# Performance work log

Hardware: AMD Instinct MI355X
Metric: run time of the kernel (lower is better)

## Reference

```python
import jax, jax.numpy as jnp
import numpy as np

N = 131072        # total nodes in batched graph
E = 2097152       # total edges (avg degree 16)
F_IN = 256        # input feature dim
DIMS = [64, 32, 16]
G = 128           # number of graphs in batch


def setup_inputs() -> dict:
    key = jax.random.key(0)
    ks = jax.random.split(key, 16)
    inp = {
        "features": jax.random.normal(ks[0], (N, F_IN), jnp.float32),
        "src": jax.random.randint(ks[1], (E,), 0, N),
        "dst": jax.random.randint(ks[2], (E,), 0, N),
        "graph_ids": jnp.sort(jax.random.randint(ks[3], (N,), 0, G)),
    }
    d = F_IN
    for i, out in enumerate(DIMS):
        inp[f"W{i}"] = jax.random.normal(ks[4 + 2 * i], (d, out), jnp.float32) / np.sqrt(d).astype(np.float32)
        inp[f"b{i}"] = jax.random.normal(ks[5 + 2 * i], (out,), jnp.float32) * 0.01
        d = out
    inp["Wc"] = jax.random.normal(ks[10], (DIMS[-1], 1), jnp.float32) / np.sqrt(DIMS[-1]).astype(np.float32)
    inp["bc"] = jax.random.normal(ks[11], (1,), jnp.float32) * 0.01
    return inp


def _graph_conv(h, W, b, src, dst, src_norm, dst_norm):
    # DGL GraphConv, norm='both', activation=relu, allow_zero_in_degree=True
    # (in_feats > out_feats everywhere here, so project before aggregating)
    hw = (h * src_norm) @ W                       # [N, out]
    agg = jax.ops.segment_sum(hw[src], dst, num_segments=N)  # gather->scatter-add
    return jax.nn.relu(agg * dst_norm + b)


def reference(features, src, dst, graph_ids, W0, b0, W1, b1, W2, b2, Wc, bc):
    ones_e = jnp.ones((E,), jnp.float32)
    out_deg = jax.ops.segment_sum(ones_e, src, num_segments=N)
    in_deg = jax.ops.segment_sum(ones_e, dst, num_segments=N)
    # DGL clamps degrees to >=1 before pow(-0.5)
    src_norm = jnp.power(jnp.maximum(out_deg, 1.0), -0.5)[:, None]  # [N,1]
    dst_norm = jnp.power(jnp.maximum(in_deg, 1.0), -0.5)[:, None]

    h = features
    for W, b in ((W0, b0), (W1, b1), (W2, b2)):
        h = _graph_conv(h, W, b, src, dst, src_norm, dst_norm)

    # dgl.mean_nodes over batched graph
    sums = jax.ops.segment_sum(h, graph_ids, num_segments=G)          # [G,16]
    cnt = jax.ops.segment_sum(jnp.ones((N,), jnp.float32), graph_ids, num_segments=G)
    hg = sums / jnp.maximum(cnt, 1.0)[:, None]

    return (hg @ Wc + bc).squeeze(-1)  # [G] logits
```

## Files before the change

### kernel.cpp

```cpp
#include <hip/hip_runtime.h>

#define N_NODES 131072
#define N_EDGES 2097152
#define N_GRAPHS 128
#define POOL_NPB 256
#define NB 256
#define BUCKET_SHIFT 9
#define BUCKET_CAP 9728
#define BIN_EPT 32

__global__ __launch_bounds__(256) void k_init_buckets(int* __restrict__ cursor_d,
                                                      int* __restrict__ cursor_s) {
  int i = threadIdx.x;
  cursor_d[i] = i * BUCKET_CAP;
  cursor_s[i] = i * BUCKET_CAP;
}

__global__ __launch_bounds__(256) void k_bin(const int* __restrict__ src,
                                             const int* __restrict__ dst,
                                             int* __restrict__ cursor_d,
                                             int* __restrict__ cursor_s,
                                             unsigned int* __restrict__ recs_d,
                                             unsigned short* __restrict__ recs_s) {
  __shared__ int hd[NB];
  __shared__ int hs[NB];
  const int t = threadIdx.x;
  const int e0 = blockIdx.x * (256 * BIN_EPT);
  hd[t] = 0; hs[t] = 0;
  __syncthreads();
#pragma unroll 4
  for (int k = 0; k < BIN_EPT; ++k) {
    int e = e0 + k * 256 + t;
    atomicAdd(&hd[dst[e] >> BUCKET_SHIFT], 1);
    atomicAdd(&hs[src[e] >> BUCKET_SHIFT], 1);
  }
  __syncthreads();
  { int c = hd[t]; hd[t] = c ? atomicAdd(&cursor_d[t], c) : 0; }
  { int c = hs[t]; hs[t] = c ? atomicAdd(&cursor_s[t], c) : 0; }
  __syncthreads();
#pragma unroll 4
  for (int k = 0; k < BIN_EPT; ++k) {
    int e = e0 + k * 256 + t;
    int s = src[e];
    int d = dst[e];
    int pd = atomicAdd(&hd[d >> BUCKET_SHIFT], 1);
    recs_d[pd] = ((unsigned int)s << BUCKET_SHIFT) | (unsigned int)(d & 511);
    int ps = atomicAdd(&hs[s >> BUCKET_SHIFT], 1);
    recs_s[ps] = (unsigned short)(s & 511);
  }
}

__global__ __launch_bounds__(512) void k_outdeg(const unsigned short* __restrict__ recs_s,
                                                const int* __restrict__ cursor_s,
                                                float* __restrict__ src_norm) {
  __shared__ int hist[512];
  const int b = blockIdx.x;
  const int t = threadIdx.x;
  hist[t] = 0;
  __syncthreads();
  const int beg = b * BUCKET_CAP;
  const int end = cursor_s[b];
  for (int i = beg + t; i < end; i += 512) atomicAdd(&hist[recs_s[i]], 1);
  __syncthreads();
  int od = hist[t]; if (od < 1) od = 1;
  src_norm[b * 512 + t] = 1.0f / sqrtf((float)od);
}

__global__ __launch_bounds__(256) void k_bucket_scan(const int* __restrict__ cursor_d,
                                                     int* __restrict__ bucket_base,
                                                     int* __restrict__ row_start) {
  __shared__ int tmp[256];
  int t = threadIdx.x;
  int c = cursor_d[t] - t * BUCKET_CAP;
  tmp[t] = c;
  __syncthreads();
  for (int off = 1; off < 256; off <<= 1) {
    int x = (t >= off) ? tmp[t - off] : 0;
    __syncthreads();
    tmp[t] += x;
    __syncthreads();
  }
  bucket_base[t] = tmp[t] - c;
  if (t == 0) row_start[N_NODES] = N_EDGES;
}

__global__ __launch_bounds__(512) void k_fill2(const unsigned int* __restrict__ recs_d,
                                               const int* __restrict__ cursor_d,
                                               const int* __restrict__ bucket_base,
                                               int* __restrict__ row_start,
                                               float* __restrict__ dst_norm,
                                               int* __restrict__ csr_src) {
  __shared__ int hist[512];
  __shared__ int lcur[512];
  const int b = blockIdx.x;
  const int t = threadIdx.x;
  hist[t] = 0;
  __syncthreads();
  const int beg = b * BUCKET_CAP;
  const int end = cursor_d[b];
  for (int i = beg + t; i < end; i += 512) atomicAdd(&hist[recs_d[i] & 511], 1);
  __syncthreads();
  int deg = hist[t];
  lcur[t] = deg;
  __syncthreads();
  for (int off = 1; off < 512; off <<= 1) {
    int x = (t >= off) ? lcur[t - off] : 0;
    __syncthreads();
    lcur[t] += x;
    __syncthreads();
  }
  int rs = bucket_base[b] + lcur[t] - deg;
  row_start[b * 512 + t] = rs;
  int dd = deg < 1 ? 1 : deg;
  dst_norm[b * 512 + t] = 1.0f / sqrtf((float)dd);
  lcur[t] = rs;
  __syncthreads();
  for (int i = beg + t; i < end; i += 512) {
    unsigned int r = recs_d[i];
    int p = atomicAdd(&lcur[r & 511], 1);
    csr_src[p] = (int)(r >> BUCKET_SHIFT);
  }
}

template <int DIN, int DOUT>
__global__ __launch_bounds__(256) void k_gemm(const float* __restrict__ h,
                                              const float* __restrict__ src_norm,
                                              const float* __restrict__ W,
                                              float* __restrict__ out) {
  constexpr int KC   = 32;
  constexpr int ROWS = 64;
  constexpr int TN   = DOUT / 16;
  constexpr int WEL  = KC * DOUT;
  __shared__ float hT[KC][ROWS];
  __shared__ float Ws[KC][DOUT];

  const int t  = threadIdx.x;
  const int rowBase = blockIdx.x * ROWS;
  const int tr = t & 15;
  const int tc = t >> 4;
  const int rg0 = (t >> 3) & 31;
  const int ph  = t >> 8;
  const int ks  = (t & 7) * 4;

  float acc[4][TN];
#pragma unroll
  for (int i = 0; i < 4; ++i)
#pragma unroll
    for (int j = 0; j < TN; ++j) acc[i][j] = 0.0f;

  for (int kc = 0; kc < DIN; kc += KC) {
#pragma unroll
    for (int p = 0; p < 2; ++p) {
      int rg = rg0 + 32 * p;
      float4 v = *reinterpret_cast<const float4*>(&h[(size_t)(rowBase + rg) * DIN + kc + ks]);
      hT[ks + 0][rg ^ ((((ks + 0) >> 3) & 3) << 3)] = v.x;
      hT[ks + 1][rg ^ ((((ks + 1) >> 3) & 3) << 3)] = v.y;
      hT[ks + 2][rg ^ ((((ks + 2) >> 3) & 3) << 3)] = v.z;
      hT[ks + 3][rg ^ ((((ks + 3) >> 3) & 3) << 3)] = v.w;
    }
#pragma unroll
    for (int base = 0; base < WEL; base += 256 * 4) {
      int idx = base + t * 4;
      if (idx < WEL)
        *reinterpret_cast<float4*>(&Ws[0][0] + idx) =
            *reinterpret_cast<const float4*>(&W[(size_t)kc * DOUT + idx]);
    }
    __syncthreads();
#pragma unroll
    for (int kk = 0; kk < KC; ++kk) {
      const int swz = ((kk >> 3) & 3) << 3;
      float4 a0 = *reinterpret_cast<const float4*>(&hT[kk][(tr * 4) ^ swz]);
      float bb[TN];
#pragma unroll
      for (int j = 0; j < TN; ++j) bb[j] = Ws[kk][tc * TN + j];
      float av[4] = {a0.x, a0.y, a0.z, a0.w};
#pragma unroll
      for (int i = 0; i < 4; ++i)
#pragma unroll
        for (int j = 0; j < TN; ++j) acc[i][j] += av[i] * bb[j];
    }
    __syncthreads();
  }

#pragma unroll
  for (int i = 0; i < 4; ++i) {
    int row = rowBase + tr * 4 + i;
    float nrm = src_norm[row];
    float* op = &out[(size_t)row * DOUT + tc * TN];
    if constexpr (TN == 4) {
      float4 v = {acc[i][0] * nrm, acc[i][1] * nrm, acc[i][2] * nrm, acc[i][3] * nrm};
      *reinterpret_cast<float4*>(op) = v;
    } else if constexpr (TN == 2) {
      float2 v = {acc[i][0] * nrm, acc[i][1] * nrm};
      *reinterpret_cast<float2*>(op) = v;
    } else {
      op[0] = acc[i][0] * nrm;
    }
  }
}

template <int D>
__global__ __launch_bounds__(256) void k_agg(const float* __restrict__ hw,
                                             const int* __restrict__ row_start,
                                             const int* __restrict__ csr_src,
                                             const float* __restrict__ dst_norm,
                                             const float* __restrict__ bias,
                                             float* __restrict__ out) {
  constexpr int LPN = D / 4;
  constexpr int NPW = 64 / LPN;
  const int t = threadIdx.x;
  const int lane = t & 63;
  const int wave = t >> 6;
  const int f4  = (lane % LPN) * 4;
  const int sub = lane / LPN;
  const int node = (blockIdx.x * 4 + wave) * NPW + sub;
  const int start = row_start[node];
  const int end   = row_start[node + 1];
  float ax = 0.0f, ay = 0.0f, az = 0.0f, aw = 0.0f;
  int i = start;
  for (; i + 4 <= end; i += 4) {
    int s0 = csr_src[i + 0];
    int s1 = csr_src[i + 1];
    int s2 = csr_src[i + 2];
    int s3 = csr_src[i + 3];
    float4 v0 = *reinterpret_cast<const float4*>(&hw[(size_t)s0 * D + f4]);
    float4 v1 = *reinterpret_cast<const float4*>(&hw[(size_t)s1 * D + f4]);
    float4 v2 = *reinterpret_cast<const float4*>(&hw[(size_t)s2 * D + f4]);
    float4 v3 = *reinterpret_cast<const float4*>(&hw[(size_t)s3 * D + f4]);
    ax += v0.x + v1.x + v2.x + v3.x;
    ay += v0.y + v1.y + v2.y + v3.y;
    az += v0.z + v1.z + v2.z + v3.z;
    aw += v0.w + v1.w + v2.w + v3.w;
  }
  for (; i < end; ++i) {
    float4 v = *reinterpret_cast<const float4*>(&hw[(size_t)csr_src[i] * D + f4]);
    ax += v.x; ay += v.y; az += v.z; aw += v.w;
  }
  float nrm = dst_norm[node];
  float4 b4 = *reinterpret_cast<const float4*>(&bias[f4]);
  float4 r;
  r.x = fmaxf(ax * nrm + b4.x, 0.0f);
  r.y = fmaxf(ay * nrm + b4.y, 0.0f);
  r.z = fmaxf(az * nrm + b4.z, 0.0f);
  r.w = fmaxf(aw * nrm + b4.w, 0.0f);
  *reinterpret_cast<float4*>(&out[(size_t)node * D + f4]) = r;
}

__global__ __launch_bounds__(256) void k_pool(const float* __restrict__ h3,
                                              const int* __restrict__ gid,
                                              float* __restrict__ sums,
                                              float* __restrict__ cnt) {
  const int t = threadIdx.x;
  const int f = t & 15;
  const int grp = t >> 4;
  const int base = blockIdx.x * POOL_NPB;
  float acc = 0.0f, c = 0.0f;
  int cur = gid[base + grp];
#pragma unroll 4
  for (int k = 0; k < POOL_NPB / 16; ++k) {
    int node = base + grp + k * 16;
    int g = gid[node];
    float v = h3[(size_t)node * 16 + f];
    if (g != cur) {
      atomicAdd(&sums[cur * 16 + f], acc);
      if (f == 0) atomicAdd(&cnt[cur], c);
      acc = 0.0f; c = 0.0f; cur = g;
    }
    acc += v; c += 1.0f;
  }
  atomicAdd(&sums[cur * 16 + f], acc);
  if (f == 0) atomicAdd(&cnt[cur], c);
}

__global__ __launch_bounds__(128) void k_classify(const float* __restrict__ sums,
                                                  const float* __restrict__ cnt,
                                                  const float* __restrict__ Wc,
                                                  const float* __restrict__ bc,
                                                  float* __restrict__ out) {
  int g = threadIdx.x;
  float c = cnt[g]; if (c < 1.0f) c = 1.0f;
  float acc = 0.0f;
#pragma unroll
  for (int f = 0; f < 16; ++f) acc += (sums[g * 16 + f] / c) * Wc[f];
  out[g] = acc + bc[0];
}

extern "C" void kernel_launch(void* const* d_in, const int* in_sizes, int n_in,
                              void* d_out, int out_size, void* d_ws, size_t ws_size,
                              hipStream_t stream) {
  const float* features = (const float*)d_in[0];
  const int*   src      = (const int*)d_in[1];
  const int*   dst      = (const int*)d_in[2];
  const int*   gid      = (const int*)d_in[3];
  const float* W0 = (const float*)d_in[4];
  const float* b0 = (const float*)d_in[5];
  const float* W1 = (const float*)d_in[6];
  const float* b1 = (const float*)d_in[7];
  const float* W2 = (const float*)d_in[8];
  const float* b2 = (const float*)d_in[9];
  const float* Wc = (const float*)d_in[10];
  const float* bc = (const float*)d_in[11];
  float* out = (float*)d_out;

  char* w = (char*)d_ws;
  auto alloc = [&](size_t bytes) {
    void* p = (void*)w;
    w += (bytes + 255) & ~(size_t)255;
    return p;
  };
  float* src_norm    = (float*)alloc((size_t)N_NODES * 4);
  float* dst_norm    = (float*)alloc((size_t)N_NODES * 4);
  int*   row_start   = (int*)alloc((size_t)(N_NODES + 1) * 4);
  int*   cursor_d    = (int*)alloc(NB * 4);
  int*   cursor_s    = (int*)alloc(NB * 4);
  int*   bucket_base = (int*)alloc(NB * 4);
  int*   csr_src     = (int*)alloc((size_t)N_EDGES * 4);
  float* buf0        = (float*)alloc((size_t)N_NODES * 64 * 4);
  float* buf1        = (float*)alloc((size_t)N_NODES * 64 * 4);
  float* sums        = (float*)alloc((size_t)N_GRAPHS * 16 * 4);
  float* cnt         = (float*)alloc((size_t)N_GRAPHS * 4);
  unsigned int*   recs_d = (unsigned int*)buf0;
  unsigned short* recs_s = (unsigned short*)buf1;

  hipMemsetAsync(sums, 0, (size_t)(N_GRAPHS * 16 + N_GRAPHS) * 4, stream);

  k_init_buckets<<<1, 256, 0, stream>>>(cursor_d, cursor_s);
  k_bin<<<N_EDGES / (256 * BIN_EPT), 256, 0, stream>>>(src, dst, cursor_d, cursor_s,
                                                       recs_d, recs_s);
  k_outdeg<<<NB, 512, 0, stream>>>(recs_s, cursor_s, src_norm);
  k_bucket_scan<<<1, 256, 0, stream>>>(cursor_d, bucket_base, row_start);
  k_fill2<<<NB, 512, 0, stream>>>(recs_d, cursor_d, bucket_base, row_start,
                                  dst_norm, csr_src);

  k_gemm<256, 64><<<N_NODES / 64, 256, 0, stream>>>(features, src_norm, W0, buf0);
  k_agg<64><<<N_NODES / 16, 256, 0, stream>>>(buf0, row_start, csr_src, dst_norm, b0, buf1);
  k_gemm<64, 32><<<N_NODES / 64, 256, 0, stream>>>(buf1, src_norm, W1, buf0);
  k_agg<32><<<N_NODES / 32, 256, 0, stream>>>(buf0, row_start, csr_src, dst_norm, b1, buf1);
  k_gemm<32, 16><<<N_NODES / 64, 256, 0, stream>>>(buf1, src_norm, W2, buf0);
  k_agg<16><<<N_NODES / 64, 256, 0, stream>>>(buf0, row_start, csr_src, dst_norm, b2, buf1);

  k_pool<<<N_NODES / POOL_NPB, 256, 0, stream>>>(buf1, gid, sums, cnt);
  k_classify<<<1, 128, 0, stream>>>(sums, cnt, Wc, bc, out);
}
```

Baseline: 343.5 us.

## Restructure GEMM to one row per lane with wave-uniform scalar W loads

```diff
diff --git a/kernel.cpp b/kernel.cpp
--- a/kernel.cpp
+++ b/kernel.cpp
@@ -129,26 +129,23 @@
                                               float* __restrict__ out) {
   constexpr int KC   = 32;
   constexpr int ROWS = 64;
-  constexpr int TN   = DOUT / 16;
-  constexpr int WEL  = KC * DOUT;
+  constexpr int NCH  = DIN / KC;
+  constexpr int CPW  = DOUT / 4;
   __shared__ float hT[KC][ROWS];
-  __shared__ float Ws[KC][DOUT];
-
-  const int t  = threadIdx.x;
+
+  const int t    = threadIdx.x;
+  const int lane = t & 63;
+  const int wv   = __builtin_amdgcn_readfirstlane(t >> 6);
   const int rowBase = blockIdx.x * ROWS;
-  const int tr = t & 15;
-  const int tc = t >> 4;
-  const int rg0 = (t >> 3) & 31;
-  const int ph  = t >> 8;
+  const int rg0 = t >> 3;
   const int ks  = (t & 7) * 4;
 
-  float acc[4][TN];
-#pragma unroll
-  for (int i = 0; i < 4; ++i)
-#pragma unroll
-    for (int j = 0; j < TN; ++j) acc[i][j] = 0.0f;
-
-  for (int kc = 0; kc < DIN; kc += KC) {
+  float acc[CPW];
+#pragma unroll
+  for (int j = 0; j < CPW; ++j) acc[j] = 0.0f;
+
+  for (int ch = 0; ch < NCH; ++ch) {
+    const int kc = ch * KC;
 #pragma unroll
     for (int p = 0; p < 2; ++p) {
       int rg = rg0 + 32 * p;
@@ -158,44 +155,27 @@
       hT[ks + 2][rg ^ ((((ks + 2) >> 3) & 3) << 3)] = v.z;
       hT[ks + 3][rg ^ ((((ks + 3) >> 3) & 3) << 3)] = v.w;
     }
-#pragma unroll
-    for (int base = 0; base < WEL; base += 256 * 4) {
-      int idx = base + t * 4;
-      if (idx < WEL)
-        *reinterpret_cast<float4*>(&Ws[0][0] + idx) =
-            *reinterpret_cast<const float4*>(&W[(size_t)kc * DOUT + idx]);
-    }
-    __syncthreads();
+    __syncthreads();
+    const float* Wrow = &W[(size_t)kc * DOUT + wv * CPW];
 #pragma unroll
     for (int kk = 0; kk < KC; ++kk) {
       const int swz = ((kk >> 3) & 3) << 3;
-      float4 a0 = *reinterpret_cast<const float4*>(&hT[kk][(tr * 4) ^ swz]);
-      float bb[TN];
-#pragma unroll
-      for (int j = 0; j < TN; ++j) bb[j] = Ws[kk][tc * TN + j];
-      float av[4] = {a0.x, a0.y, a0.z, a0.w};
-#pragma unroll
-      for (int i = 0; i < 4; ++i)
-#pragma unroll
-        for (int j = 0; j < TN; ++j) acc[i][j] += av[i] * bb[j];
+      float a = hT[kk][lane ^ swz];
+#pragma unroll
+      for (int j = 0; j < CPW; ++j)
+        acc[j] += a * Wrow[kk * DOUT + j];
     }
     __syncthreads();
   }
 
-#pragma unroll
-  for (int i = 0; i < 4; ++i) {
-    int row = rowBase + tr * 4 + i;
-    float nrm = src_norm[row];
-    float* op = &out[(size_t)row * DOUT + tc * TN];
-    if constexpr (TN == 4) {
-      float4 v = {acc[i][0] * nrm, acc[i][1] * nrm, acc[i][2] * nrm, acc[i][3] * nrm};
-      *reinterpret_cast<float4*>(op) = v;
-    } else if constexpr (TN == 2) {
-      float2 v = {acc[i][0] * nrm, acc[i][1] * nrm};
-      *reinterpret_cast<float2*>(op) = v;
-    } else {
-      op[0] = acc[i][0] * nrm;
-    }
+  const int row = rowBase + lane;
+  float nrm = src_norm[row];
+  float* op = &out[(size_t)row * DOUT + wv * CPW];
+#pragma unroll
+  for (int q = 0; q < CPW / 4; ++q) {
+    float4 v = {acc[q * 4 + 0] * nrm, acc[q * 4 + 1] * nrm,
+                acc[q * 4 + 2] * nrm, acc[q * 4 + 3] * nrm};
+    *reinterpret_cast<float4*>(op + q * 4) = v;
   }
 }
 
```

Result: no change. 339.2 us (-1.2%).
